# Kernel tuning notes

Measured on AMD Instinct MI355X. Metric: run time of the kernel, lower is better.

Reference implementation:

```python
import jax, jax.numpy as jnp
import numpy as np
import math

NUM_HEADS = 16
HEAD_DIM = 64
DIM = 1024
IO_SLOTS = 16
NEG_INF = 1.0e9


def _alibi_slopes(num_heads):
    # slopes = ratio**i for i in 1..n, ratio = 2**(-8/n)
    ratio = 2.0 ** (-8.0 / num_heads)
    return jnp.array([ratio ** i for i in range(1, num_heads + 1)], dtype=jnp.float32)


def setup_inputs() -> dict:
    key = jax.random.key(0)
    ks = jax.random.split(key, 7)
    B, S, D = 2, 2048, DIM
    x = jax.random.normal(ks[0], (B, S, D), dtype=jnp.float32)
    is_getchar = jax.random.uniform(ks[1], (B, S), dtype=jnp.float32)
    is_putchar = jax.random.uniform(ks[2], (B, S), dtype=jnp.float32)
    scale = 0.02
    wq = jax.random.normal(ks[3], (D, NUM_HEADS * HEAD_DIM), dtype=jnp.float32) * scale
    wk = jax.random.normal(ks[4], (D, NUM_HEADS * HEAD_DIM), dtype=jnp.float32) * scale
    wv = jax.random.normal(ks[5], (D, NUM_HEADS * HEAD_DIM), dtype=jnp.float32) * scale
    wo = jax.random.normal(ks[6], (NUM_HEADS * HEAD_DIM, D), dtype=jnp.float32) * scale
    return {"x": x, "is_getchar": is_getchar, "is_putchar": is_putchar,
            "wq": wq, "wk": wk, "wv": wv, "wo": wo}


def reference(x, is_getchar, is_putchar, wq, wk, wv, wo):
    B, S, D = x.shape
    H, hd = NUM_HEADS, HEAD_DIM
    io_start = D - IO_SLOTS

    q = (x @ wq).reshape(B, S, H, hd)
    k = (x @ wk).reshape(B, S, H, hd)
    v = (x @ wv).reshape(B, S, H, hd)

    # scores[b,h,i,j] = q . k / sqrt(hd)
    scores = jnp.einsum("bihd,bjhd->bhij", q, k) / math.sqrt(hd)

    # standard ALiBi bias: -slope * (i - j), causal masked
    positions = jnp.arange(S)
    dist = (positions[:, None] - positions[None, :]).astype(jnp.float32)  # [S,S] = i - j
    slopes = _alibi_slopes(H)  # [H]
    bias = -slopes[:, None, None] * dist  # [H,S,S]
    causal = jnp.triu(jnp.ones((S, S), dtype=jnp.float32), k=1)
    bias = bias - causal * NEG_INF
    scores = scores + bias[None]

    # targeted read-head bias on head 0: -slope0 * |target - j|
    read_anchor = x[..., io_start + 0]  # [B,S]
    read_offset = x[..., io_start + 1]  # [B,S]
    target = read_anchor + 1.0 + read_offset  # [B,S]
    read_bias = -slopes[0] * jnp.abs(target[..., None] - positions.astype(jnp.float32))  # [B,S,S]
    head0 = jnp.where(is_getchar[:, None, :, None] > 0.5, read_bias[:, None], scores[:, :1])
    scores = scores.at[:, :1].set(head0)

    attn = jax.nn.softmax(scores, axis=-1)
    attn_out = jnp.einsum("bhij,bjhd->bihd", attn, v).reshape(B, S, H * hd)
    output = x + attn_out @ wo

    # I/O state updates (last 16 channels)
    output = output.at[..., io_start + 1].add(is_getchar)   # read_offset += getchar
    output = output.at[..., io_start + 3].add(is_putchar)   # write_offset += putchar
    output = output.at[..., io_start + 13].set(is_putchar)  # output_ready = putchar
    return output
```

## Files before the change

kernel.cpp:

```cpp
#include <hip/hip_runtime.h>
#include <hip/hip_bf16.h>

typedef __hip_bfloat16 bf16;
typedef __attribute__((ext_vector_type(8))) short short8;
typedef __attribute__((ext_vector_type(4))) short short4v;
typedef __attribute__((ext_vector_type(4))) float f32x4;

#define MFMA16(a, b, c) __builtin_amdgcn_mfma_f32_16x16x32_bf16((a), (b), (c), 0, 0, 0)

#if __has_builtin(__builtin_amdgcn_mfma_f32_16x16x16bf16_1k)
#define MFMA_PV(a, b, c) __builtin_amdgcn_mfma_f32_16x16x16bf16_1k((a), (b), (c), 0, 0, 0)
#elif __has_builtin(__builtin_amdgcn_mfma_f32_16x16x16_bf16)
#define MFMA_PV(a, b, c) __builtin_amdgcn_mfma_f32_16x16x16_bf16((a), (b), (c), 0, 0, 0)
#else
static __device__ __forceinline__ f32x4 mfma_pv_asm(short4v a, short4v b, f32x4 c) {
    f32x4 d;
    asm volatile("v_mfma_f32_16x16x16_bf16 %0, %1, %2, %3"
                 : "=&v"(d) : "v"(a), "v"(b), "v"(c));
    return d;
}
#define MFMA_PV(a, b, c) mfma_pv_asm((a), (b), (c))
#endif

static __device__ __forceinline__ void gload_lds16(const bf16* g, bf16* l) {
    __builtin_amdgcn_global_load_lds((const __attribute__((address_space(1))) void*)g,
                                     (__attribute__((address_space(3))) void*)l, 16, 0, 0);
}

__global__ __launch_bounds__(256) void cast_x_kernel(const float* __restrict__ in,
                                                     bf16* __restrict__ out) {
    int i = (blockIdx.x * 256 + threadIdx.x) * 4;
    float4 v = *(const float4*)(in + i);
    union { bf16 h4[4]; uint2 u; } p;
    p.h4[0] = __float2bfloat16(v.x);
    p.h4[1] = __float2bfloat16(v.y);
    p.h4[2] = __float2bfloat16(v.z);
    p.h4[3] = __float2bfloat16(v.w);
    *(uint2*)(out + i) = p.u;
}

__global__ __launch_bounds__(256) void transpose_cast_kernel(
    const float* __restrict__ wq, const float* __restrict__ wk,
    const float* __restrict__ wv, const float* __restrict__ wo,
    bf16* __restrict__ WqkvT, bf16* __restrict__ WoT) {
    __shared__ bf16 tile[64][65];
    int bid = blockIdx.x;
    int mat = bid >> 8;
    int t   = bid & 255;
    int tn  = t >> 4, tk = t & 15;
    const float* src = (mat == 0) ? wq : (mat == 1) ? wk : (mat == 2) ? wv : wo;
    bf16* dst = (mat < 3) ? (WqkvT + (size_t)mat * 1024 * 1024) : WoT;
    int tx = threadIdx.x & 63, ty = threadIdx.x >> 6;
    int k0 = tk * 64, n0 = tn * 64;
#pragma unroll
    for (int p = 0; p < 16; ++p) {
        int r = p * 4 + ty;
        tile[r][tx] = __float2bfloat16(src[(size_t)(k0 + r) * 1024 + n0 + tx]);
    }
    __syncthreads();
#pragma unroll
    for (int p = 0; p < 16; ++p) {
        int r = p * 4 + ty;
        dst[(size_t)(n0 + r) * 1024 + k0 + tx] = tile[tx][r];
    }
}

__global__ __launch_bounds__(256) void gemm_qkv_kernel(
    const bf16* __restrict__ A, const bf16* __restrict__ Bt,
    bf16* __restrict__ QK, bf16* __restrict__ Vt) {
    const int K = 1024;
    int bm = blockIdx.x, bn = blockIdx.y;
    __shared__ bf16 As[128 * 32];
    __shared__ bf16 Bs[128 * 32];
    int tid = threadIdx.x;
    int lane = tid & 63, w = tid >> 6;
    int wm = (w >> 1) * 64, wn = (w & 1) * 64;
    int q4 = lane >> 4, li = lane & 15;
    int srow = tid >> 2, sc = (tid & 3) * 8;

    const bf16* Ag = A + (size_t)(bm * 128 + srow) * K + sc;
    const bf16* Bg = Bt + (size_t)(bn * 128 + srow) * K + sc;
    bf16* Asl = As + tid * 8;
    bf16* Asl2 = As + 2048 + tid * 8;
    bf16* Bsl = Bs + tid * 8;
    bf16* Bsl2 = Bs + 2048 + tid * 8;

    f32x4 acc[4][4];
#pragma unroll
    for (int mt = 0; mt < 4; ++mt)
#pragma unroll
        for (int nt = 0; nt < 4; ++nt) acc[mt][nt] = (f32x4){0.f, 0.f, 0.f, 0.f};

    for (int k0 = 0; k0 < K; k0 += 32) {
        __syncthreads();
        gload_lds16(Ag + k0, Asl);
        gload_lds16(Ag + 64 * K + k0, Asl2);
        gload_lds16(Bg + k0, Bsl);
        gload_lds16(Bg + 64 * K + k0, Bsl2);
        __syncthreads();
        short8 af[4], bfb[4];
#pragma unroll
        for (int mt = 0; mt < 4; ++mt)
            af[mt] = *(const short8*)(As + (wm + mt * 16 + li) * 32 + q4 * 8);
#pragma unroll
        for (int nt = 0; nt < 4; ++nt)
            bfb[nt] = *(const short8*)(Bs + (wn + nt * 16 + li) * 32 + q4 * 8);
#pragma unroll
        for (int mt = 0; mt < 4; ++mt)
#pragma unroll
            for (int nt = 0; nt < 4; ++nt)
                acc[mt][nt] = MFMA16(af[mt], bfb[nt], acc[mt][nt]);
    }

    int rowb = bm * 128 + wm;
    if (bn < 16) {
#pragma unroll
        for (int mt = 0; mt < 4; ++mt) {
#pragma unroll
            for (int nt = 0; nt < 4; ++nt) {
                int col = bn * 128 + wn + nt * 16 + li;
#pragma unroll
                for (int r = 0; r < 4; ++r) {
                    int row = rowb + mt * 16 + q4 * 4 + r;
                    QK[(size_t)row * 2048 + col] = __float2bfloat16(acc[mt][nt][r]);
                }
            }
        }
    } else {
#pragma unroll
        for (int mt = 0; mt < 4; ++mt) {
            int sbase = rowb + mt * 16 + q4 * 4;
            int b = sbase >> 11, s = sbase & 2047;
#pragma unroll
            for (int nt = 0; nt < 4; ++nt) {
                int n = bn * 128 + wn + nt * 16 + li - 2048;
                int h = n >> 6, d = n & 63;
                union { bf16 h4[4]; uint2 u; } pk;
#pragma unroll
                for (int r = 0; r < 4; ++r) pk.h4[r] = __float2bfloat16(acc[mt][nt][r]);
                *(uint2*)(Vt + (size_t)((b * 16 + h) * 64 + d) * 2048 + s) = pk.u;
            }
        }
    }
}

__global__ __launch_bounds__(256, 3) void attn_kernel(
    const bf16* __restrict__ QK, const bf16* __restrict__ Vt,
    const float* __restrict__ x, const float* __restrict__ gch,
    bf16* __restrict__ AO) {
    const int S = 2048;
    int idx = blockIdx.x;
    int ti, h, b;
    if (idx < 64) { h = 0; b = idx & 1; ti = idx >> 1; }
    else {
        int i2 = idx - 64;
        int row = i2 / 30;
        int j = i2 - row * 30;
        ti = 31 - row; h = 1 + (j >> 1); b = j & 1;
    }
    int i0 = ti * 64;
    int tid = threadIdx.x, lane = tid & 63, w = tid >> 6;
    int q4 = lane >> 4, li = lane & 15;

    __shared__ bf16 Ks[64 * 72];
    __shared__ bf16 Vs[64 * 72];
    __shared__ float Ored[64 * 68];
    __shared__ float lsumBuf[4][64];

    short8 qf[4][2];
#pragma unroll
    for (int it = 0; it < 4; ++it) {
        const bf16* qp = QK + (size_t)(b * S + i0 + it * 16 + li) * 2048 + h * 64 + q4 * 8;
        qf[it][0] = *(const short8*)(qp);
        qf[it][1] = *(const short8*)(qp + 32);
    }

    const float L2E = 1.4426950408889634f;
    float slope = exp2f(-0.5f * (float)(h + 1));
    float s1  = 0.125f * L2E;
    float sl1 = slope * L2E;
    const float slope0_1 = 0.70710678118654752f * L2E;

    float tgt[4]; int gcm[4];
    if (h == 0) {
#pragma unroll
        for (int it = 0; it < 4; ++it) {
            size_t ix = (size_t)(b * S + i0 + it * 16 + li);
            gcm[it] = gch[ix] > 0.5f ? 1 : 0;
            tgt[it] = x[ix * 1024 + 1008] + 1.0f + x[ix * 1024 + 1009];
        }
    } else {
#pragma unroll
        for (int it = 0; it < 4; ++it) { gcm[it] = 0; tgt[it] = 0.f; }
    }

    float lsum[4] = {0.f, 0.f, 0.f, 0.f};
    f32x4 o[4][4];
#pragma unroll
    for (int it = 0; it < 4; ++it)
#pragma unroll
        for (int dt = 0; dt < 4; ++dt) o[it][dt] = (f32x4){0.f, 0.f, 0.f, 0.f};

    int srow = tid >> 3, scv = (tid & 7) * 8;
    const bf16* Kg = QK + (size_t)(b * S + srow) * 2048 + 1024 + h * 64 + scv;
    const bf16* Vg = Vt + (size_t)((b * 16 + h) * 64 + srow) * 2048 + scv;

    int ntiles = (h == 0) ? (S / 64) : (ti + 1);
    for (int jt = 0; jt < ntiles; ++jt) {
        int j0 = jt * 64;
        uint4 kv0 = *(const uint4*)(Kg + (size_t)j0 * 2048);
        uint4 kv1 = *(const uint4*)(Kg + (size_t)(j0 + 32) * 2048);
        uint4 vv0 = *(const uint4*)(Vg + j0);
        uint4 vv1 = *(const uint4*)(Vg + (size_t)32 * 2048 + j0);
        __syncthreads();
        *(uint4*)(Ks + srow * 72 + scv) = kv0;
        *(uint4*)(Ks + (srow + 32) * 72 + scv) = kv1;
        *(uint4*)(Vs + srow * 72 + scv) = vv0;
        *(uint4*)(Vs + (srow + 32) * 72 + scv) = vv1;
        __syncthreads();

        short8 kf0 = *(const short8*)(Ks + (w * 16 + li) * 72 + q4 * 8);
        short8 kf1 = *(const short8*)(Ks + (w * 16 + li) * 72 + 32 + q4 * 8);
        f32x4 sAcc[4];
#pragma unroll
        for (int it = 0; it < 4; ++it) {
            f32x4 z = (f32x4){0.f, 0.f, 0.f, 0.f};
            z = MFMA16(kf0, qf[it][0], z);
            z = MFMA16(kf1, qf[it][1], z);
            sAcc[it] = z;
        }

        float jbase = (float)(j0 + w * 16 + q4 * 4);
        int maskable = (jt >= ti);
        short4v pf[4];
#pragma unroll
        for (int it = 0; it < 4; ++it) {
            float fi = (float)(i0 + it * 16 + li);
            float d0 = jbase - fi;
            union { bf16 hh[4]; short4v v; } pu;
#pragma unroll
            for (int r = 0; r < 4; ++r) {
                float dj = d0 + (float)r;
                float s = fmaf(sl1, dj, sAcc[it][r] * s1);
                float p;
                if (h == 0) {
                    float jj = jbase + (float)r;
                    float sg = -slope0_1 * fabsf(tgt[it] - jj);
                    s = gcm[it] ? sg : s;
                    bool msk = (!gcm[it]) && (dj > 0.f);
                    p = msk ? 0.f : exp2f(s);
                } else {
                    p = exp2f(s);
                    if (maskable && dj > 0.f) p = 0.f;
                }
                lsum[it] += p;
                pu.hh[r] = __float2bfloat16(p);
            }
            pf[it] = pu.v;
        }

#pragma unroll
        for (int dt = 0; dt < 4; ++dt) {
            short4v vf = *(const short4v*)(Vs + (dt * 16 + li) * 72 + w * 16 + q4 * 4);
#pragma unroll
            for (int it = 0; it < 4; ++it)
                o[it][dt] = MFMA_PV(pf[it], vf, o[it][dt]);
        }
    }

#pragma unroll
    for (int it = 0; it < 4; ++it) {
        lsum[it] += __shfl_xor(lsum[it], 16, 64);
        lsum[it] += __shfl_xor(lsum[it], 32, 64);
    }
    if (lane < 16) {
#pragma unroll
        for (int it = 0; it < 4; ++it) lsumBuf[w][it * 16 + lane] = lsum[it];
    }

    __syncthreads();
    if (w == 0) {
#pragma unroll
        for (int it = 0; it < 4; ++it)
#pragma unroll
            for (int dt = 0; dt < 4; ++dt)
#pragma unroll
                for (int r = 0; r < 4; ++r)
                    Ored[(it * 16 + q4 * 4 + r) * 68 + dt * 16 + li] = o[it][dt][r];
    }
    __syncthreads();
    if (w == 1) {
#pragma unroll
        for (int it = 0; it < 4; ++it)
#pragma unroll
            for (int dt = 0; dt < 4; ++dt)
#pragma unroll
                for (int r = 0; r < 4; ++r)
                    Ored[(it * 16 + q4 * 4 + r) * 68 + dt * 16 + li] += o[it][dt][r];
    }
    __syncthreads();
    if (w == 2) {
#pragma unroll
        for (int it = 0; it < 4; ++it)
#pragma unroll
            for (int dt = 0; dt < 4; ++dt)
#pragma unroll
                for (int r = 0; r < 4; ++r)
                    Ored[(it * 16 + q4 * 4 + r) * 68 + dt * 16 + li] += o[it][dt][r];
    }
    __syncthreads();
    if (w == 3) {
#pragma unroll
        for (int it = 0; it < 4; ++it)
#pragma unroll
            for (int dt = 0; dt < 4; ++dt)
#pragma unroll
                for (int r = 0; r < 4; ++r)
                    Ored[(it * 16 + q4 * 4 + r) * 68 + dt * 16 + li] += o[it][dt][r];
    }
    __syncthreads();

    int i = tid >> 2, dseg = (tid & 3) * 16;
    float ls = lsumBuf[0][i] + lsumBuf[1][i] + lsumBuf[2][i] + lsumBuf[3][i];
    float inv = 1.0f / ls;
    bf16* dst = AO + (size_t)(b * S + i0 + i) * 1024 + h * 64 + dseg;
    union { bf16 hh[16]; uint4 u[2]; } ou;
#pragma unroll
    for (int c = 0; c < 16; ++c)
        ou.hh[c] = __float2bfloat16(Ored[i * 68 + dseg + c] * inv);
    *(uint4*)(dst) = ou.u[0];
    *(uint4*)(dst + 8) = ou.u[1];
}

__global__ __launch_bounds__(256) void gemm_out_kernel(
    const bf16* __restrict__ A, const bf16* __restrict__ Bt,
    const float* __restrict__ x, float* __restrict__ out) {
    const int K = 1024;
    int bm = blockIdx.x, bn = blockIdx.y;
    __shared__ bf16 As[128 * 32];
    __shared__ bf16 Bs[128 * 32];
    int tid = threadIdx.x;
    int lane = tid & 63, w = tid >> 6;
    int wm = (w >> 1) * 64, wn = (w & 1) * 64;
    int q4 = lane >> 4, li = lane & 15;
    int srow = tid >> 2, sc = (tid & 3) * 8;

    const bf16* Ag = A + (size_t)(bm * 128 + srow) * K + sc;
    const bf16* Bg = Bt + (size_t)(bn * 128 + srow) * K + sc;
    bf16* Asl = As + tid * 8;
    bf16* Asl2 = As + 2048 + tid * 8;
    bf16* Bsl = Bs + tid * 8;
    bf16* Bsl2 = Bs + 2048 + tid * 8;

    f32x4 acc[4][4];
#pragma unroll
    for (int mt = 0; mt < 4; ++mt)
#pragma unroll
        for (int nt = 0; nt < 4; ++nt) acc[mt][nt] = (f32x4){0.f, 0.f, 0.f, 0.f};

    for (int k0 = 0; k0 < K; k0 += 32) {
        __syncthreads();
        gload_lds16(Ag + k0, Asl);
        gload_lds16(Ag + 64 * K + k0, Asl2);
        gload_lds16(Bg + k0, Bsl);
        gload_lds16(Bg + 64 * K + k0, Bsl2);
        __syncthreads();
        short8 af[4], bfb[4];
#pragma unroll
        for (int mt = 0; mt < 4; ++mt)
            af[mt] = *(const short8*)(As + (wm + mt * 16 + li) * 32 + q4 * 8);
#pragma unroll
        for (int nt = 0; nt < 4; ++nt)
            bfb[nt] = *(const short8*)(Bs + (wn + nt * 16 + li) * 32 + q4 * 8);
#pragma unroll
        for (int mt = 0; mt < 4; ++mt)
#pragma unroll
            for (int nt = 0; nt < 4; ++nt)
                acc[mt][nt] = MFMA16(af[mt], bfb[nt], acc[mt][nt]);
    }

#pragma unroll
    for (int mt = 0; mt < 4; ++mt) {
#pragma unroll
        for (int nt = 0; nt < 4; ++nt) {
            int col = bn * 128 + wn + nt * 16 + li;
#pragma unroll
            for (int r = 0; r < 4; ++r) {
                int row = bm * 128 + wm + mt * 16 + q4 * 4 + r;
                size_t idx = (size_t)row * 1024 + col;
                out[idx] = x[idx] + acc[mt][nt][r];
            }
        }
    }
}

__global__ __launch_bounds__(256) void io_fix_kernel(float* __restrict__ out,
                                                     const float* __restrict__ gch,
                                                     const float* __restrict__ pch) {
    int r = blockIdx.x * 256 + threadIdx.x;
    float g = gch[r], p = pch[r];
    size_t base = (size_t)r * 1024;
    out[base + 1009] += g;
    out[base + 1011] += p;
    out[base + 1021] = p;
}

extern "C" void kernel_launch(void* const* d_in, const int* in_sizes, int n_in,
                              void* d_out, int out_size, void* d_ws, size_t ws_size,
                              hipStream_t stream) {
    (void)in_sizes; (void)n_in; (void)out_size; (void)ws_size;
    const float* x   = (const float*)d_in[0];
    const float* gch = (const float*)d_in[1];
    const float* pch = (const float*)d_in[2];
    const float* wq  = (const float*)d_in[3];
    const float* wk  = (const float*)d_in[4];
    const float* wv  = (const float*)d_in[5];
    const float* wo  = (const float*)d_in[6];
    float* out = (float*)d_out;

    char* ws = (char*)d_ws;
    bf16* Xb    = (bf16*)(ws);
    bf16* WqkvT = (bf16*)(ws + (size_t)( 8 << 20));
    bf16* WoT   = (bf16*)(ws + (size_t)(14 << 20));
    bf16* QK    = (bf16*)(ws + (size_t)(16 << 20));
    bf16* Vt    = (bf16*)(ws + (size_t)(32 << 20));
    bf16* AO    = Xb;

    cast_x_kernel<<<4096, 256, 0, stream>>>(x, Xb);
    transpose_cast_kernel<<<1024, 256, 0, stream>>>(wq, wk, wv, wo, WqkvT, WoT);
    gemm_qkv_kernel<<<dim3(32, 24), 256, 0, stream>>>(Xb, WqkvT, QK, Vt);
    attn_kernel<<<1024, 256, 0, stream>>>(QK, Vt, x, gch, AO);
    gemm_out_kernel<<<dim3(32, 8), 256, 0, stream>>>(AO, WoT, x, out);
    io_fix_kernel<<<16, 256, 0, stream>>>(out, gch, pch);
}
```

Measured before the change: 205.3 us.

## Double-buffer K/V tiles in LDS with register prefetch in attention loop

New measurement: 204.0 us (median of 2 runs). No clear change (-0.6%).

```diff
diff --git a/kernel.cpp b/kernel.cpp
--- a/kernel.cpp
+++ b/kernel.cpp
@@ -162,10 +162,11 @@
     int tid = threadIdx.x, lane = tid & 63, w = tid >> 6;
     int q4 = lane >> 4, li = lane & 15;
 
-    __shared__ bf16 Ks[64 * 72];
-    __shared__ bf16 Vs[64 * 72];
-    __shared__ float Ored[64 * 68];
-    __shared__ float lsumBuf[4][64];
+    __shared__ __align__(16) char smem[36864];
+    bf16* KsB = (bf16*)smem;
+    bf16* VsB = (bf16*)(smem + 18432);
+    float* Ored = (float*)smem;
+    float* lsumBuf = (float*)(smem + 17408);
 
     short8 qf[4][2];
 #pragma unroll
@@ -206,18 +207,33 @@
     const bf16* Vg = Vt + (size_t)((b * 16 + h) * 64 + srow) * 2048 + scv;
 
     int ntiles = (h == 0) ? (S / 64) : (ti + 1);
+
+    {
+        uint4 kv0 = *(const uint4*)(Kg);
+        uint4 kv1 = *(const uint4*)(Kg + (size_t)32 * 2048);
+        uint4 vv0 = *(const uint4*)(Vg);
+        uint4 vv1 = *(const uint4*)(Vg + (size_t)32 * 2048);
+        *(uint4*)(KsB + srow * 72 + scv) = kv0;
+        *(uint4*)(KsB + (srow + 32) * 72 + scv) = kv1;
+        *(uint4*)(VsB + srow * 72 + scv) = vv0;
+        *(uint4*)(VsB + (srow + 32) * 72 + scv) = vv1;
+    }
+    __syncthreads();
+
+    int cur = 0;
     for (int jt = 0; jt < ntiles; ++jt) {
         int j0 = jt * 64;
-        uint4 kv0 = *(const uint4*)(Kg + (size_t)j0 * 2048);
-        uint4 kv1 = *(const uint4*)(Kg + (size_t)(j0 + 32) * 2048);
-        uint4 vv0 = *(const uint4*)(Vg + j0);
-        uint4 vv1 = *(const uint4*)(Vg + (size_t)32 * 2048 + j0);
-        __syncthreads();
-        *(uint4*)(Ks + srow * 72 + scv) = kv0;
-        *(uint4*)(Ks + (srow + 32) * 72 + scv) = kv1;
-        *(uint4*)(Vs + srow * 72 + scv) = vv0;
-        *(uint4*)(Vs + (srow + 32) * 72 + scv) = vv1;
-        __syncthreads();
+        uint4 nk0, nk1, nv0, nv1;
+        bool pref = (jt + 1 < ntiles);
+        if (pref) {
+            int jn = j0 + 64;
+            nk0 = *(const uint4*)(Kg + (size_t)jn * 2048);
+            nk1 = *(const uint4*)(Kg + (size_t)(jn + 32) * 2048);
+            nv0 = *(const uint4*)(Vg + jn);
+            nv1 = *(const uint4*)(Vg + (size_t)32 * 2048 + jn);
+        }
+        const bf16* Ks = KsB + cur * 4608;
+        const bf16* Vs = VsB + cur * 4608;
 
         short8 kf0 = *(const short8*)(Ks + (w * 16 + li) * 72 + q4 * 8);
         short8 kf1 = *(const short8*)(Ks + (w * 16 + li) * 72 + 32 + q4 * 8);
@@ -266,6 +282,17 @@
             for (int it = 0; it < 4; ++it)
                 o[it][dt] = MFMA_PV(pf[it], vf, o[it][dt]);
         }
+
+        if (pref) {
+            bf16* Kn = KsB + (cur ^ 1) * 4608;
+            bf16* Vn = VsB + (cur ^ 1) * 4608;
+            *(uint4*)(Kn + srow * 72 + scv) = nk0;
+            *(uint4*)(Kn + (srow + 32) * 72 + scv) = nk1;
+            *(uint4*)(Vn + srow * 72 + scv) = nv0;
+            *(uint4*)(Vn + (srow + 32) * 72 + scv) = nv1;
+        }
+        __syncthreads();
+        cur ^= 1;
     }
 
 #pragma unroll
@@ -275,7 +302,7 @@
     }
     if (lane < 16) {
 #pragma unroll
-        for (int it = 0; it < 4; ++it) lsumBuf[w][it * 16 + lane] = lsum[it];
+        for (int it = 0; it < 4; ++it) lsumBuf[w * 64 + it * 16 + lane] = lsum[it];
     }
 
     __syncthreads();
@@ -321,7 +348,7 @@
     __syncthreads();
 
     int i = tid >> 2, dseg = (tid & 3) * 16;
-    float ls = lsumBuf[0][i] + lsumBuf[1][i] + lsumBuf[2][i] + lsumBuf[3][i];
+    float ls = lsumBuf[0 * 64 + i] + lsumBuf[1 * 64 + i] + lsumBuf[2 * 64 + i] + lsumBuf[3 * 64 + i];
     float inv = 1.0f / ls;
     bf16* dst = AO + (size_t)(b * S + i0 + i) * 1024 + h * 64 + dseg;
     union { bf16 hh[16]; uint4 u[2]; } ou;
```
